# Kernel optimization log

Hardware: AMD Instinct MI355X
Metric: run time of the kernel (lower is better)

## Reference

```python
import jax, jax.numpy as jnp
import numpy as np

T = 4096       # sentence length
E = 256        # embedding_dim
H = 512        # hidden_dim (bidirectional total)
HD = H // 2    # per-direction hidden
V = 100000     # vocab_size
NT = 16        # tagset_size
START, STOP = 14, 15
NEG = -10000.0


def setup_inputs() -> dict:
    key = jax.random.key(0)
    ks = jax.random.split(key, 20)
    sentence = jax.random.randint(ks[0], (T,), 0, V)
    emb = jax.random.normal(ks[1], (V, E), dtype=jnp.float32)
    # PyTorch LSTM params: gate order [i, f, g, o], weight_ih [4*HD, E], weight_hh [4*HD, HD]
    s = 1.0 / np.sqrt(HD)
    def U(k, shape):
        return jax.random.uniform(k, shape, dtype=jnp.float32, minval=-s, maxval=s)
    Wih_f, Whh_f = U(ks[2], (4 * HD, E)), U(ks[3], (4 * HD, HD))
    bih_f, bhh_f = U(ks[4], (4 * HD,)), U(ks[5], (4 * HD,))
    Wih_b, Whh_b = U(ks[6], (4 * HD, E)), U(ks[7], (4 * HD, HD))
    bih_b, bhh_b = U(ks[8], (4 * HD,)), U(ks[9], (4 * HD,))
    h0 = jax.random.normal(ks[10], (2, 1, HD), dtype=jnp.float32)  # init_hidden()
    c0 = jax.random.normal(ks[11], (2, 1, HD), dtype=jnp.float32)
    # attention params (zeros in the original; small randn for a non-degenerate baseline)
    w_omega = jax.random.normal(ks[12], (H, H), dtype=jnp.float32) * 0.01
    u_omega = jax.random.normal(ks[13], (H,), dtype=jnp.float32) * 0.01
    sl = 1.0 / np.sqrt(H)
    W_tag = jax.random.uniform(ks[14], (NT, H), dtype=jnp.float32, minval=-sl, maxval=sl)
    b_tag = jax.random.uniform(ks[15], (NT,), dtype=jnp.float32, minval=-sl, maxval=sl)
    transitions = jax.random.normal(ks[16], (NT, NT), dtype=jnp.float32)
    transitions = transitions.at[START, :].set(NEG).at[:, STOP].set(NEG)
    return dict(sentence=sentence, emb=emb,
                Wih_f=Wih_f, Whh_f=Whh_f, bih_f=bih_f, bhh_f=bhh_f,
                Wih_b=Wih_b, Whh_b=Whh_b, bih_b=bih_b, bhh_b=bhh_b,
                h0=h0, c0=c0, w_omega=w_omega, u_omega=u_omega,
                W_tag=W_tag, b_tag=b_tag, transitions=transitions)


def _lstm_dir(x, h0, c0, Wih, Whh, bih, bhh, reverse):
    # x: [T, E]; returns hidden states [T, HD]
    def step(carry, xt):
        h, c = carry
        g = xt @ Wih.T + h @ Whh.T + bih + bhh  # [4*HD]
        i, f, gg, o = jnp.split(g, 4)
        i, f, o = jax.nn.sigmoid(i), jax.nn.sigmoid(f), jax.nn.sigmoid(o)
        c = f * c + i * jnp.tanh(gg)
        h = o * jnp.tanh(c)
        return (h, c), h
    _, hs = jax.lax.scan(step, (h0, c0), x, reverse=reverse)
    return hs


def _lstm_feats(sentence, emb, Wih_f, Whh_f, bih_f, bhh_f,
                Wih_b, Whh_b, bih_b, bhh_b, h0, c0,
                w_omega, u_omega, W_tag, b_tag):
    x = emb[sentence]  # [T, E]
    hf = _lstm_dir(x, h0[0, 0], c0[0, 0], Wih_f, Whh_f, bih_f, bhh_f, False)
    hb = _lstm_dir(x, h0[1, 0], c0[1, 0], Wih_b, Whh_b, bih_b, bhh_b, True)
    out = jnp.concatenate([hf, hb], axis=-1)  # [T, H] (lstm_out with batch=1 squeezed)
    # attention_net: softmax over time of a scalar score per position
    logits = jnp.tanh(out @ w_omega) @ u_omega  # [T]
    alphas = jax.nn.softmax(logits)
    attn_out = out * alphas[:, None]  # [T, H]
    return attn_out @ W_tag.T + b_tag  # [T, NT]


def _viterbi(feats, transitions):
    init = jnp.full((NT,), NEG, dtype=feats.dtype).at[START].set(0.0)
    def step(fv, feat):
        scores = fv[None, :] + transitions  # [next_tag, prev_tag]
        bp = jnp.argmax(scores, axis=1)
        return jnp.max(scores, axis=1) + feat, bp
    fv, bps = jax.lax.scan(step, init, feats)
    terminal = fv + transitions[STOP]
    best = jnp.argmax(terminal)
    score = terminal[best]
    def back(tag, bp):
        return bp[tag], tag
    _, path = jax.lax.scan(back, best, bps, reverse=True)  # path[t] = best tag at t
    return score, path


def reference(sentence, emb, Wih_f, Whh_f, bih_f, bhh_f,
              Wih_b, Whh_b, bih_b, bhh_b, h0, c0,
              w_omega, u_omega, W_tag, b_tag, transitions):
    feats = _lstm_feats(sentence, emb, Wih_f, Whh_f, bih_f, bhh_f,
                        Wih_b, Whh_b, bih_b, bhh_b, h0, c0,
                        w_omega, u_omega, W_tag, b_tag)
    score, path = _viterbi(feats, transitions)
    return score, path
```

## Files before the change

kernel.cpp:

```cpp
#include <hip/hip_runtime.h>
#include <hip/hip_fp16.h>

#define T_LEN 4096
#define START_TAG 14
#define STOP_TAG 15
#define NEG_VAL -10000.0f

typedef unsigned int u32;
typedef unsigned short u16;
typedef unsigned long long u64;
typedef int v4i __attribute__((ext_vector_type(4)));

#define GX_OFF      0u
#define OUT_OFF     16777216u
#define LOGITS_OFF  25165824u
#define ALPHAS_OFF  25182208u
#define FEATS_OFF   25198592u
#define CMAT_OFF    25460736u
#define VIN_OFF     25591808u
#define BP_OFF      25600000u
#define BMAP_OFF    25632768u
#define STAIL_OFF   25640960u
#define BEST_OFF    25649152u

__device__ __forceinline__ u32 packq(int q0, int q1, int q2, int q3) {
  return (u32)(q0 & 255) | ((u32)(q1 & 255) << 8) |
         ((u32)(q2 & 255) << 16) | ((u32)(q3 & 255) << 24);
}

__device__ __forceinline__ float sigm(float x) {
  return __builtin_amdgcn_rcpf(1.f + __expf(-x));
}
__device__ __forceinline__ float tanh_fast(float x) {
  float e = __expf(-2.f * fabsf(x));
  float r = (1.f - e) * __builtin_amdgcn_rcpf(1.f + e);
  return copysignf(r, x);
}

__global__ void prep_kernel(float* logits) {
  const int i = threadIdx.x + blockIdx.x * 1024;
  if (i < 4096) logits[i] = 0.f;
}

__global__ __launch_bounds__(256) void gx_kernel(
    const int* __restrict__ sentence, const float* __restrict__ emb,
    const float* __restrict__ Wih_f, const float* __restrict__ Wih_b,
    const float* __restrict__ bih_f, const float* __restrict__ bhh_f,
    const float* __restrict__ bih_b, const float* __restrict__ bhh_b,
    __half* __restrict__ Gx)
{
  __shared__ float ws[32][260];
  const int r0 = blockIdx.x * 32;
  const int t0 = blockIdx.y * 32;
  const int tid = threadIdx.x;
  {
    const int c4 = (tid & 63) * 4;
    const int rA = tid >> 6;
    #pragma unroll
    for (int p = 0; p < 8; ++p) {
      const int rr = rA + p * 4;
      const int R = r0 + rr;
      const float* src = (R < 1024) ? (Wih_f + (size_t)R * 256 + c4)
                                    : (Wih_b + (size_t)(R - 1024) * 256 + c4);
      *(float4*)&ws[rr][c4] = *(const float4*)src;
    }
  }
  __syncthreads();
  const int ttb = tid >> 4, rgb = tid & 15;
  const int s0r = sentence[t0 + ttb];
  const int s1r = sentence[t0 + ttb + 16];
  const float* x0p = emb + (size_t)s0r * 256;
  const float* x1p = emb + (size_t)s1r * 256;
  float acc00 = 0, acc01 = 0, acc10 = 0, acc11 = 0;
  #pragma unroll 4
  for (int c4 = 0; c4 < 256; c4 += 4) {
    float4 x0 = *(const float4*)(x0p + c4);
    float4 x1 = *(const float4*)(x1p + c4);
    float4 w0 = *(const float4*)&ws[rgb][c4];
    float4 w1 = *(const float4*)&ws[rgb + 16][c4];
    acc00 += x0.x*w0.x + x0.y*w0.y + x0.z*w0.z + x0.w*w0.w;
    acc01 += x0.x*w1.x + x0.y*w1.y + x0.z*w1.z + x0.w*w1.w;
    acc10 += x1.x*w0.x + x1.y*w0.y + x1.z*w0.z + x1.w*w0.w;
    acc11 += x1.x*w1.x + x1.y*w1.y + x1.z*w1.z + x1.w*w1.w;
  }
  #pragma unroll
  for (int ri = 0; ri < 2; ++ri) {
    const int R = r0 + rgb + ri * 16;
    const int dir = R >> 10, grow = R & 1023;
    const int gate = grow >> 8, dd = grow & 255;
    const float bias = dir ? (bih_b[grow] + bhh_b[grow])
                           : (bih_f[grow] + bhh_f[grow]);
    const float a0 = ri ? acc01 : acc00;
    const float a1 = ri ? acc11 : acc10;
    const size_t off = (size_t)dir * 1024 + dd * 4 + gate;
    Gx[(size_t)(t0 + ttb) * 2048 + off]      = __float2half(a0 + bias);
    Gx[(size_t)(t0 + ttb + 16) * 2048 + off] = __float2half(a1 + bias);
  }
}

__global__ __launch_bounds__(512, 2) void lstm_kernel(
    const float* __restrict__ Whh_f, const float* __restrict__ Whh_b,
    const float* __restrict__ h0, const float* __restrict__ c0,
    const __half* __restrict__ Gx, float* __restrict__ out_lstm)
{
  const int dir = blockIdx.x;
  const int tid = threadIdx.x;
  const int w = tid >> 6, l = tid & 63;
  const int mr = l & 15, q = l >> 4;
  const float* Whh = dir ? Whh_b : Whh_f;

  __shared__ __align__(16) char hq8[2][256];
  __shared__ __align__(16) int graw[1024];
  __shared__ float fsh[1024];
  __shared__ __align__(16) u16 hist[128 * 256];

  v4i wfrag[8][4];
  #pragma unroll
  for (int m = 0; m < 8; ++m) {
    const int row = 128 * w + 16 * m + mr;
    const float* wr = Whh + (size_t)row * 256 + 16 * q;
    float mx = 1e-10f;
    #pragma unroll
    for (int t = 0; t < 4; ++t) {
      #pragma unroll
      for (int c4 = 0; c4 < 4; ++c4) {
        float4 f = *(const float4*)(wr + 64 * t + 4 * c4);
        mx = fmaxf(mx, fmaxf(fmaxf(fabsf(f.x), fabsf(f.y)),
                             fmaxf(fabsf(f.z), fabsf(f.w))));
      }
    }
    mx = fmaxf(mx, __shfl_xor(mx, 16));
    mx = fmaxf(mx, __shfl_xor(mx, 32));
    const float qs = 127.f / mx;
    if (q == 0) fsh[row] = mx * (1.f / (127.f * 32.f));
    #pragma unroll
    for (int t = 0; t < 4; ++t) {
      u32 pk[4];
      #pragma unroll
      for (int c4 = 0; c4 < 4; ++c4) {
        float4 f = *(const float4*)(wr + 64 * t + 4 * c4);
        pk[c4] = packq((int)rintf(f.x * qs), (int)rintf(f.y * qs),
                       (int)rintf(f.z * qs), (int)rintf(f.w * qs));
      }
      v4i v; v[0] = (int)pk[0]; v[1] = (int)pk[1]; v[2] = (int)pk[2]; v[3] = (int)pk[3];
      wfrag[m][t] = v;
    }
  }

  float creg = 0.f;
  if (tid < 256) {
    creg = c0[dir * 256 + tid];
    float hv = h0[dir * 256 + tid];
    int qq = max(-127, min(127, (int)rintf(hv * 32.f)));
    hq8[0][tid] = (char)qq;
  }
  __syncthreads();

  float fsi = 0.f, fsf = 0.f, fsg = 0.f, fso = 0.f;
  if (tid < 256) {
    fsi = fsh[tid]; fsf = fsh[256 + tid];
    fsg = fsh[512 + tid]; fso = fsh[768 + tid];
  }
  const uint2* Gx2 = (const uint2*)Gx;

  for (int sb = 0; sb < T_LEN; sb += 16) {
    uint2 gb[16];
    if (tid < 256) {
      #pragma unroll
      for (int k = 0; k < 16; ++k) {
        const int t = dir ? (T_LEN - 1 - (sb + k)) : (sb + k);
        gb[k] = Gx2[(size_t)t * 512 + dir * 256 + tid];
      }
    }
    #pragma unroll
    for (int k = 0; k < 16; ++k) {
      const int s = sb + k;
      const char* hc = hq8[k & 1];
      v4i bfr[4];
      #pragma unroll
      for (int t = 0; t < 4; ++t)
        bfr[t] = *(const v4i*)(hc + 64 * t + 16 * q);
      #pragma unroll
      for (int m = 0; m < 8; ++m) {
        v4i acc; acc[0] = 0; acc[1] = 0; acc[2] = 0; acc[3] = 0;
        acc = __builtin_amdgcn_mfma_i32_16x16x64_i8(wfrag[m][0], bfr[0], acc, 0, 0, 0);
        acc = __builtin_amdgcn_mfma_i32_16x16x64_i8(wfrag[m][1], bfr[1], acc, 0, 0, 0);
        acc = __builtin_amdgcn_mfma_i32_16x16x64_i8(wfrag[m][2], bfr[2], acc, 0, 0, 0);
        acc = __builtin_amdgcn_mfma_i32_16x16x64_i8(wfrag[m][3], bfr[3], acc, 0, 0, 0);
        if (mr == 0)
          *(v4i*)&graw[128 * w + 16 * m + 4 * q] = acc;
      }
      __syncthreads();
      if (tid < 256) {
        const int d = tid;
        const int ri = graw[d],        rf = graw[256 + d];
        const int rg = graw[512 + d],  ro = graw[768 + d];
        const float xi = (float)ri * fsi + __half2float(__ushort_as_half((u16)(gb[k].x & 0xffff)));
        const float xf = (float)rf * fsf + __half2float(__ushort_as_half((u16)(gb[k].x >> 16)));
        const float xg = (float)rg * fsg + __half2float(__ushort_as_half((u16)(gb[k].y & 0xffff)));
        const float xo = (float)ro * fso + __half2float(__ushort_as_half((u16)(gb[k].y >> 16)));
        const float iv = sigm(xi);
        const float fv = sigm(xf);
        const float gv = tanh_fast(xg);
        const float ov = sigm(xo);
        creg = __builtin_fmaf(fv, creg, iv * gv);
        const float h = ov * tanh_fast(creg);
        hist[(s & 127) * 256 + d] = __half_as_ushort(__float2half(h));
        int qq = max(-127, min(127, (int)rintf(h * 32.f)));
        hq8[(k + 1) & 1][d] = (char)qq;
      }
      __syncthreads();
      if ((s & 127) == 127) {
        const int sbase = s - 127;
        #pragma unroll 4
        for (int i = 0; i < 16; ++i) {
          const int idx = tid + i * 512;
          const int step = idx >> 6, d0 = (idx & 63) * 4;
          const int tt = sbase + step;
          const int tg = dir ? (T_LEN - 1 - tt) : tt;
          uint2 hv = ((const uint2*)hist)[idx];
          float4 ov4;
          ov4.x = __half2float(__ushort_as_half((u16)(hv.x & 0xffff)));
          ov4.y = __half2float(__ushort_as_half((u16)(hv.x >> 16)));
          ov4.z = __half2float(__ushort_as_half((u16)(hv.y & 0xffff)));
          ov4.w = __half2float(__ushort_as_half((u16)(hv.y >> 16)));
          *(float4*)&out_lstm[(size_t)tg * 512 + dir * 256 + d0] = ov4;
        }
        __syncthreads();
      }
    }
  }
}

__global__ __launch_bounds__(256) void attn_kernel(
    const float* __restrict__ out_lstm, const float* __restrict__ w_omega,
    const float* __restrict__ u_omega, float* __restrict__ logits)
{
  __shared__ float bst[32][132];
  const int c0 = blockIdx.x * 32;
  const int t0 = blockIdx.y * 32;
  const int tid = threadIdx.x;
  const int ttb = tid >> 4, cgb = tid & 15;
  const float* a0p = out_lstm + (size_t)(t0 + ttb) * 512;
  const float* a1p = out_lstm + (size_t)(t0 + ttb + 16) * 512;
  float acc00 = 0, acc01 = 0, acc10 = 0, acc11 = 0;
  for (int kh = 0; kh < 4; ++kh) {
    __syncthreads();
    {
      const int cc = tid & 31;
      const int kA = tid >> 5;
      #pragma unroll
      for (int p = 0; p < 16; ++p) {
        const int kkx = kA + p * 8;
        bst[cc][kkx] = w_omega[(size_t)(kh * 128 + kkx) * 512 + c0 + cc];
      }
    }
    __syncthreads();
    #pragma unroll 4
    for (int k4 = 0; k4 < 128; k4 += 4) {
      float4 a0 = *(const float4*)(a0p + kh * 128 + k4);
      float4 a1 = *(const float4*)(a1p + kh * 128 + k4);
      float4 b0 = *(const float4*)&bst[cgb][k4];
      float4 b1 = *(const float4*)&bst[cgb + 16][k4];
      acc00 += a0.x*b0.x + a0.y*b0.y + a0.z*b0.z + a0.w*b0.w;
      acc01 += a0.x*b1.x + a0.y*b1.y + a0.z*b1.z + a0.w*b1.w;
      acc10 += a1.x*b0.x + a1.y*b0.y + a1.z*b0.z + a1.w*b0.w;
      acc11 += a1.x*b1.x + a1.y*b1.y + a1.z*b1.z + a1.w*b1.w;
    }
  }
  const float u0 = u_omega[c0 + cgb], u1 = u_omega[c0 + 16 + cgb];
  float s0 = tanh_fast(acc00) * u0 + tanh_fast(acc01) * u1;
  float s1 = tanh_fast(acc10) * u0 + tanh_fast(acc11) * u1;
  #pragma unroll
  for (int msk = 1; msk < 16; msk <<= 1) {
    s0 += __shfl_xor(s0, msk);
    s1 += __shfl_xor(s1, msk);
  }
  if (cgb == 0) {
    atomicAdd(&logits[t0 + ttb], s0);
    atomicAdd(&logits[t0 + ttb + 16], s1);
  }
}

__global__ __launch_bounds__(1024) void softmax_kernel(
    const float* __restrict__ logits, float* __restrict__ alphas)
{
  __shared__ float red[1024];
  const int tid = threadIdx.x;
  float l0 = logits[tid], l1 = logits[1024 + tid];
  float l2 = logits[2048 + tid], l3 = logits[3072 + tid];
  red[tid] = fmaxf(fmaxf(l0, l1), fmaxf(l2, l3));
  __syncthreads();
  for (int s = 512; s > 0; s >>= 1) {
    if (tid < s) red[tid] = fmaxf(red[tid], red[tid + s]);
    __syncthreads();
  }
  const float gm = red[0];
  __syncthreads();
  float e0 = __expf(l0 - gm), e1 = __expf(l1 - gm);
  float e2 = __expf(l2 - gm), e3 = __expf(l3 - gm);
  red[tid] = e0 + e1 + e2 + e3;
  __syncthreads();
  for (int s = 512; s > 0; s >>= 1) {
    if (tid < s) red[tid] += red[tid + s];
    __syncthreads();
  }
  const float inv = 1.0f / red[0];
  alphas[tid] = e0 * inv; alphas[1024 + tid] = e1 * inv;
  alphas[2048 + tid] = e2 * inv; alphas[3072 + tid] = e3 * inv;
}

__global__ __launch_bounds__(256) void feats_kernel(
    const float* __restrict__ out_lstm, const float* __restrict__ W_tag,
    const float* __restrict__ b_tag, const float* __restrict__ alphas,
    float* __restrict__ feats)
{
  __shared__ float wt[16][516];
  const int t0 = blockIdx.x * 16;
  const int tid = threadIdx.x;
  {
    const int k4 = (tid & 127) * 4;
    const int gA = tid >> 7;
    #pragma unroll
    for (int p = 0; p < 8; ++p) {
      const int tg = gA + p * 2;
      *(float4*)&wt[tg][k4] = *(const float4*)(W_tag + (size_t)tg * 512 + k4);
    }
  }
  __syncthreads();
  const int tt = tid >> 4, tg = tid & 15;
  const float* ap = out_lstm + (size_t)(t0 + tt) * 512;
  float acc = 0.f;
  #pragma unroll 4
  for (int k4 = 0; k4 < 512; k4 += 4) {
    float4 a = *(const float4*)(ap + k4);
    float4 b = *(const float4*)&wt[tg][k4];
    acc += a.x*b.x + a.y*b.y + a.z*b.z + a.w*b.w;
  }
  feats[(size_t)(t0 + tt) * 16 + tg] = acc * alphas[t0 + tt] + b_tag[tg];
}

__global__ __launch_bounds__(256) void vit_block_mats(
    const float* __restrict__ feats, const float* __restrict__ trans,
    float* __restrict__ Cmat)
{
  __shared__ float C[2][16][17];
  const int b = blockIdx.x;
  const int tid = threadIdx.x;
  const int n = tid >> 4, p = tid & 15;
  float tr[16];
  #pragma unroll
  for (int k = 0; k < 16; ++k) tr[k] = trans[n * 16 + k];
  const int t0 = b * 32;
  C[0][n][p] = tr[p] + feats[t0 * 16 + n];
  float fnext = feats[(t0 + 1) * 16 + n];
  __syncthreads();
  for (int s = 1; s < 32; ++s) {
    const float ft = fnext;
    if (s + 1 < 32) fnext = feats[(t0 + s + 1) * 16 + n];
    const int pr = (s - 1) & 1, cu = s & 1;
    float m = tr[0] + C[pr][0][p];
    #pragma unroll
    for (int k = 1; k < 16; ++k) m = fmaxf(m, tr[k] + C[pr][k][p]);
    C[cu][n][p] = m + ft;
    __syncthreads();
  }
  Cmat[b * 256 + n * 16 + p] = C[1][n][p];
}

__global__ __launch_bounds__(64) void vit_scan(
    const float* __restrict__ Cmat, const float* __restrict__ trans,
    float* __restrict__ v_in, float* __restrict__ d_out, u32* __restrict__ best_ws)
{
  const int l = threadIdx.x;
  const int n = l & 15, pg = l >> 4;
  float v = (n == START_TAG) ? 0.f : NEG_VAL;
  for (int b = 0; b < 128; ++b) {
    if (pg == 0) v_in[b * 16 + n] = v;
    float4 c4 = *(const float4*)&Cmat[b * 256 + n * 16 + pg * 4];
    float cand = c4.x + __shfl(v, pg * 4 + 0);
    cand = fmaxf(cand, c4.y + __shfl(v, pg * 4 + 1));
    cand = fmaxf(cand, c4.z + __shfl(v, pg * 4 + 2));
    cand = fmaxf(cand, c4.w + __shfl(v, pg * 4 + 3));
    cand = fmaxf(cand, __shfl_xor(cand, 16));
    cand = fmaxf(cand, __shfl_xor(cand, 32));
    v = cand;
  }
  float term = v + trans[STOP_TAG * 16 + n];
  int mi = n;
  #pragma unroll
  for (int msk = 1; msk < 16; msk <<= 1) {
    float om = __shfl_xor(term, msk); int omi = __shfl_xor(mi, msk);
    if (om > term || (om == term && omi < mi)) { term = om; mi = omi; }
  }
  if (l == 0) { d_out[0] = term; *best_ws = (u32)mi; }
}

__global__ __launch_bounds__(64) void vit_bp(
    const float* __restrict__ feats, const float* __restrict__ trans,
    const float* __restrict__ v_in, u32* __restrict__ bp)
{
  const int b = blockIdx.x;
  const int l = threadIdx.x;
  const int n = l & 15, pg = l >> 4;
  const float4 tr4 = *(const float4*)&trans[n * 16 + pg * 4];
  float v = v_in[b * 16 + n];
  const int t0 = b * 32;
  float fcur = feats[t0 * 16 + n];
  for (int s = 0; s < 32; ++s) {
    const int t = t0 + s;
    float fnext = (s + 1 < 32) ? feats[(t + 1) * 16 + n] : 0.f;
    float f0 = __shfl(v, pg * 4 + 0), f1 = __shfl(v, pg * 4 + 1);
    float f2 = __shfl(v, pg * 4 + 2), f3 = __shfl(v, pg * 4 + 3);
    float m = f0 + tr4.x; int mi = pg * 4;
    float c;
    c = f1 + tr4.y; if (c > m) { m = c; mi = pg * 4 + 1; }
    c = f2 + tr4.z; if (c > m) { m = c; mi = pg * 4 + 2; }
    c = f3 + tr4.w; if (c > m) { m = c; mi = pg * 4 + 3; }
    float om; int omi;
    om = __shfl_xor(m, 16); omi = __shfl_xor(mi, 16);
    if (om > m || (om == m && omi < mi)) { m = om; mi = omi; }
    om = __shfl_xor(m, 32); omi = __shfl_xor(mi, 32);
    if (om > m || (om == m && omi < mi)) { m = om; mi = omi; }
    u32 w = (l < 16) ? ((u32)mi << ((n & 7) * 4)) : 0u;
    w |= __shfl_xor(w, 1); w |= __shfl_xor(w, 2); w |= __shfl_xor(w, 4);
    if (l == 0) bp[t * 2] = w;
    if (l == 8) bp[t * 2 + 1] = w;
    v = m + fcur;
    fcur = fnext;
  }
}

__global__ __launch_bounds__(64) void vit_bmap(
    const u32* __restrict__ bp, u32* __restrict__ Bmap)
{
  const int b = blockIdx.x;
  const int l = threadIdx.x;
  if (l >= 16) return;
  int t = b * 32 + 31;
  u32 lo = bp[t * 2], hi = bp[t * 2 + 1];
  int A = (int)(((l < 8 ? lo : hi) >> ((l & 7) * 4)) & 15u);
  for (t = b * 32 + 30; t >= b * 32; --t) {
    lo = bp[t * 2]; hi = bp[t * 2 + 1];
    A = (int)(((A < 8 ? lo : hi) >> ((A & 7) * 4)) & 15u);
  }
  Bmap[b * 16 + l] = (u32)A;
}

__global__ __launch_bounds__(64) void vit_suffix(
    const u32* __restrict__ Bmap, u32* __restrict__ Stail)
{
  __shared__ u32 bm[2048];
  const int l = threadIdx.x;
  for (int i = l; i < 2048; i += 64) bm[i] = Bmap[i];
  __syncthreads();
  if (l < 16) {
    int S = l;
    for (int b = 127; b >= 0; --b) {
      Stail[b * 16 + l] = (u32)S;
      S = (int)bm[b * 16 + S];
    }
  }
}

__global__ __launch_bounds__(64) void vit_emit(
    const u32* __restrict__ bp, const u32* __restrict__ Stail,
    const u32* __restrict__ best_ws, float* __restrict__ d_out)
{
  const int b = blockIdx.x;
  const int l = threadIdx.x;
  const int best = (int)*best_ws;
  int A = (l < 16) ? (int)Stail[b * 16 + l] : 0;
  for (int s = 31; s >= 0; --s) {
    const int t = b * 32 + s;
    const int pv = __shfl(A, best);
    if (l == 0) d_out[1 + t] = (float)pv;
    if (s > 0) {
      const u32 lo = bp[t * 2], hi = bp[t * 2 + 1];
      A = (int)(((A < 8 ? lo : hi) >> ((A & 7) * 4)) & 15u);
    }
  }
}

extern "C" void kernel_launch(void* const* d_in, const int* in_sizes, int n_in,
                              void* d_out, int out_size, void* d_ws, size_t ws_size,
                              hipStream_t stream)
{
  const int*   sentence = (const int*)  d_in[0];
  const float* emb      = (const float*)d_in[1];
  const float* Wih_f    = (const float*)d_in[2];
  const float* Whh_f    = (const float*)d_in[3];
  const float* bih_f    = (const float*)d_in[4];
  const float* bhh_f    = (const float*)d_in[5];
  const float* Wih_b    = (const float*)d_in[6];
  const float* Whh_b    = (const float*)d_in[7];
  const float* bih_b    = (const float*)d_in[8];
  const float* bhh_b    = (const float*)d_in[9];
  const float* h0       = (const float*)d_in[10];
  const float* c0       = (const float*)d_in[11];
  const float* w_omega  = (const float*)d_in[12];
  const float* u_omega  = (const float*)d_in[13];
  const float* W_tag    = (const float*)d_in[14];
  const float* b_tag    = (const float*)d_in[15];
  const float* trans    = (const float*)d_in[16];

  char* ws = (char*)d_ws;
  __half* Gx      = (__half*)(ws + GX_OFF);
  float* out_lstm = (float*)(ws + OUT_OFF);
  float* logits   = (float*)(ws + LOGITS_OFF);
  float* alphas   = (float*)(ws + ALPHAS_OFF);
  float* feats    = (float*)(ws + FEATS_OFF);
  float* Cmat     = (float*)(ws + CMAT_OFF);
  float* v_in     = (float*)(ws + VIN_OFF);
  u32*   bp       = (u32*)  (ws + BP_OFF);
  u32*   Bmap     = (u32*)  (ws + BMAP_OFF);
  u32*   Stail    = (u32*)  (ws + STAIL_OFF);
  u32*   best_ws  = (u32*)  (ws + BEST_OFF);
  float* out      = (float*)d_out;

  hipLaunchKernelGGL(prep_kernel, dim3(4), dim3(1024), 0, stream, logits);
  hipLaunchKernelGGL(gx_kernel, dim3(64, 128), dim3(256), 0, stream,
                     sentence, emb, Wih_f, Wih_b, bih_f, bhh_f, bih_b, bhh_b, Gx);
  hipLaunchKernelGGL(lstm_kernel, dim3(2), dim3(512), 0, stream,
                     Whh_f, Whh_b, h0, c0, Gx, out_lstm);
  hipLaunchKernelGGL(attn_kernel, dim3(16, 128), dim3(256), 0, stream,
                     out_lstm, w_omega, u_omega, logits);
  hipLaunchKernelGGL(softmax_kernel, dim3(1), dim3(1024), 0, stream, logits, alphas);
  hipLaunchKernelGGL(feats_kernel, dim3(256), dim3(256), 0, stream,
                     out_lstm, W_tag, b_tag, alphas, feats);
  hipLaunchKernelGGL(vit_block_mats, dim3(128), dim3(256), 0, stream,
                     feats, trans, Cmat);
  hipLaunchKernelGGL(vit_scan, dim3(1), dim3(64), 0, stream,
                     Cmat, trans, v_in, out, best_ws);
  hipLaunchKernelGGL(vit_bp, dim3(128), dim3(64), 0, stream,
                     feats, trans, v_in, bp);
  hipLaunchKernelGGL(vit_bmap, dim3(128), dim3(64), 0, stream, bp, Bmap);
  hipLaunchKernelGGL(vit_suffix, dim3(1), dim3(64), 0, stream, Bmap, Stail);
  hipLaunchKernelGGL(vit_emit, dim3(128), dim3(64), 0, stream,
                     bp, Stail, best_ws, out);
}
```

Measured before the change: 4.076 ms.

## Split LSTM gates: MFMA for i/f, per-thread sdot4 for g/o with 256 threads

The recurrent LSTM kernel drops from 512 to 256 threads per direction. The i and f gate matvecs still run on int8 MFMA. The g and o gate rows are quantized into per-thread registers (128 ints) and computed with sdot4 dot products over the broadcast h vector. Gx prefetch is double-buffered in chunks of 8 steps, and the barriers use a custom s_barrier with an explicit lgkmcnt wait. The aim is to cut barrier cost with fewer waves and overlap the MFMA work with scalar dot work, but the large per-thread register arrays risk spills and longer serial dot chains.

```diff
diff --git a/kernel.cpp b/kernel.cpp
--- a/kernel.cpp
+++ b/kernel.cpp
@@ -35,6 +35,27 @@
   float e = __expf(-2.f * fabsf(x));
   float r = (1.f - e) * __builtin_amdgcn_rcpf(1.f + e);
   return copysignf(r, x);
+}
+
+#if defined(__has_builtin)
+#  if __has_builtin(__builtin_amdgcn_sdot4)
+#    define DOT4(a, b, c) __builtin_amdgcn_sdot4((a), (b), (c), false)
+#  endif
+#endif
+#ifndef DOT4
+__device__ __forceinline__ int dot4_emu(int a, int b, int c) {
+  #pragma unroll
+  for (int j = 0; j < 4; ++j)
+    c += (int)((signed char)(a >> (8 * j))) * (int)((signed char)(b >> (8 * j)));
+  return c;
+}
+#  define DOT4(a, b, c) dot4_emu((a), (b), (c))
+#endif
+
+__device__ __forceinline__ void wg_barrier() {
+  asm volatile("s_waitcnt lgkmcnt(0)" ::: "memory");
+  __builtin_amdgcn_s_barrier();
+  __builtin_amdgcn_sched_barrier(0);
 }
 
 __global__ void prep_kernel(float* logits) {
@@ -98,20 +119,21 @@
   }
 }
 
-__global__ __launch_bounds__(512, 2) void lstm_kernel(
+__global__ __launch_bounds__(256, 1) void lstm_kernel(
     const float* __restrict__ Whh_f, const float* __restrict__ Whh_b,
     const float* __restrict__ h0, const float* __restrict__ c0,
     const __half* __restrict__ Gx, float* __restrict__ out_lstm)
 {
   const int dir = blockIdx.x;
   const int tid = threadIdx.x;
+  const int d = tid;
   const int w = tid >> 6, l = tid & 63;
   const int mr = l & 15, q = l >> 4;
   const float* Whh = dir ? Whh_b : Whh_f;
 
   __shared__ __align__(16) char hq8[2][256];
-  __shared__ __align__(16) int graw[1024];
-  __shared__ float fsh[1024];
+  __shared__ __align__(16) int graw[512];
+  __shared__ float fsh[512];
   __shared__ __align__(16) u16 hist[128 * 256];
 
   v4i wfrag[8][4];
@@ -147,39 +169,68 @@
     }
   }
 
-  float creg = 0.f;
-  if (tid < 256) {
-    creg = c0[dir * 256 + tid];
-    float hv = h0[dir * 256 + tid];
+  int wq2[2][64];
+  float fsg = 0.f, fso = 0.f;
+  #pragma unroll
+  for (int g = 0; g < 2; ++g) {
+    const float* wr = Whh + (size_t)((2 + g) * 256 + d) * 256;
+    float mx = 1e-10f;
+    #pragma unroll
+    for (int c4 = 0; c4 < 64; ++c4) {
+      float4 f = *(const float4*)(wr + c4 * 4);
+      mx = fmaxf(mx, fmaxf(fmaxf(fabsf(f.x), fabsf(f.y)),
+                           fmaxf(fabsf(f.z), fabsf(f.w))));
+    }
+    const float qs = 127.f / mx;
+    const float sc = mx * (1.f / (127.f * 32.f));
+    if (g == 0) fsg = sc; else fso = sc;
+    #pragma unroll
+    for (int c4 = 0; c4 < 64; ++c4) {
+      float4 f = *(const float4*)(wr + c4 * 4);
+      wq2[g][c4] = (int)packq((int)rintf(f.x * qs), (int)rintf(f.y * qs),
+                              (int)rintf(f.z * qs), (int)rintf(f.w * qs));
+    }
+  }
+
+  float creg = c0[dir * 256 + d];
+  {
+    float hv = h0[dir * 256 + d];
     int qq = max(-127, min(127, (int)rintf(hv * 32.f)));
-    hq8[0][tid] = (char)qq;
-  }
-  __syncthreads();
-
-  float fsi = 0.f, fsf = 0.f, fsg = 0.f, fso = 0.f;
-  if (tid < 256) {
-    fsi = fsh[tid]; fsf = fsh[256 + tid];
-    fsg = fsh[512 + tid]; fso = fsh[768 + tid];
-  }
+    hq8[0][d] = (char)qq;
+  }
+  __syncthreads();
+
+  const float fsi = fsh[d], fsf = fsh[256 + d];
   const uint2* Gx2 = (const uint2*)Gx;
-
-  for (int sb = 0; sb < T_LEN; sb += 16) {
-    uint2 gb[16];
-    if (tid < 256) {
-      #pragma unroll
-      for (int k = 0; k < 16; ++k) {
-        const int t = dir ? (T_LEN - 1 - (sb + k)) : (sb + k);
-        gb[k] = Gx2[(size_t)t * 512 + dir * 256 + tid];
-      }
-    }
-    #pragma unroll
-    for (int k = 0; k < 16; ++k) {
+  uint2 ga[8];
+  #pragma unroll
+  for (int k = 0; k < 8; ++k) {
+    const int t = dir ? (T_LEN - 1 - k) : k;
+    ga[k] = Gx2[(size_t)t * 512 + dir * 256 + d];
+  }
+
+  for (int sb = 0; sb < T_LEN; sb += 8) {
+    uint2 gn[8];
+    const bool more = (sb + 8) < T_LEN;
+    if (more) {
+      #pragma unroll
+      for (int k = 0; k < 8; ++k) {
+        const int t2 = sb + 8 + k;
+        const int t = dir ? (T_LEN - 1 - t2) : t2;
+        gn[k] = Gx2[(size_t)t * 512 + dir * 256 + d];
+      }
+    }
+    #pragma unroll
+    for (int k = 0; k < 8; ++k) {
       const int s = sb + k;
-      const char* hc = hq8[k & 1];
+      const char* hc = hq8[s & 1];
       v4i bfr[4];
       #pragma unroll
       for (int t = 0; t < 4; ++t)
         bfr[t] = *(const v4i*)(hc + 64 * t + 16 * q);
+      int4 hv[16];
+      #pragma unroll
+      for (int c = 0; c < 16; ++c) hv[c] = ((const int4*)hc)[c];
       #pragma unroll
       for (int m = 0; m < 8; ++m) {
         v4i acc; acc[0] = 0; acc[1] = 0; acc[2] = 0; acc[3] = 0;
@@ -190,44 +241,60 @@
         if (mr == 0)
           *(v4i*)&graw[128 * w + 16 * m + 4 * q] = acc;
       }
-      __syncthreads();
-      if (tid < 256) {
-        const int d = tid;
-        const int ri = graw[d],        rf = graw[256 + d];
-        const int rg = graw[512 + d],  ro = graw[768 + d];
-        const float xi = (float)ri * fsi + __half2float(__ushort_as_half((u16)(gb[k].x & 0xffff)));
-        const float xf = (float)rf * fsf + __half2float(__ushort_as_half((u16)(gb[k].x >> 16)));
-        const float xg = (float)rg * fsg + __half2float(__ushort_as_half((u16)(gb[k].y & 0xffff)));
-        const float xo = (float)ro * fso + __half2float(__ushort_as_half((u16)(gb[k].y >> 16)));
-        const float iv = sigm(xi);
-        const float fv = sigm(xf);
-        const float gv = tanh_fast(xg);
-        const float ov = sigm(xo);
-        creg = __builtin_fmaf(fv, creg, iv * gv);
-        const float h = ov * tanh_fast(creg);
-        hist[(s & 127) * 256 + d] = __half_as_ushort(__float2half(h));
+      int ag0 = 0, ag1 = 0, ao0 = 0, ao1 = 0;
+      #pragma unroll
+      for (int c = 0; c < 16; ++c) {
+        const int4 h4 = hv[c];
+        ag0 = DOT4(wq2[0][4*c+0], h4.x, ag0);
+        ao0 = DOT4(wq2[1][4*c+0], h4.x, ao0);
+        ag1 = DOT4(wq2[0][4*c+1], h4.y, ag1);
+        ao1 = DOT4(wq2[1][4*c+1], h4.y, ao1);
+        ag0 = DOT4(wq2[0][4*c+2], h4.z, ag0);
+        ao0 = DOT4(wq2[1][4*c+2], h4.z, ao0);
+        ag1 = DOT4(wq2[0][4*c+3], h4.w, ag1);
+        ao1 = DOT4(wq2[1][4*c+3], h4.w, ao1);
+      }
+      const int ag = ag0 + ag1, ao = ao0 + ao1;
+      wg_barrier();
+      const int ri = graw[d], rf = graw[256 + d];
+      const float xi = (float)ri * fsi + __half2float(__ushort_as_half((u16)(ga[k].x & 0xffff)));
+      const float xf = (float)rf * fsf + __half2float(__ushort_as_half((u16)(ga[k].x >> 16)));
+      const float xg = (float)ag * fsg + __half2float(__ushort_as_half((u16)(ga[k].y & 0xffff)));
+      const float xo = (float)ao * fso + __half2float(__ushort_as_half((u16)(ga[k].y >> 16)));
+      const float iv = sigm(xi);
+      const float fv = sigm(xf);
+      const float gv = tanh_fast(xg);
+      const float ov = sigm(xo);
+      creg = __builtin_fmaf(fv, creg, iv * gv);
+      const float h = ov * tanh_fast(creg);
+      {
         int qq = max(-127, min(127, (int)rintf(h * 32.f)));
-        hq8[(k + 1) & 1][d] = (char)qq;
-      }
-      __syncthreads();
-      if ((s & 127) == 127) {
-        const int sbase = s - 127;
-        #pragma unroll 4
-        for (int i = 0; i < 16; ++i) {
-          const int idx = tid + i * 512;
-          const int step = idx >> 6, d0 = (idx & 63) * 4;
-          const int tt = sbase + step;
-          const int tg = dir ? (T_LEN - 1 - tt) : tt;
-          uint2 hv = ((const uint2*)hist)[idx];
-          float4 ov4;
-          ov4.x = __half2float(__ushort_as_half((u16)(hv.x & 0xffff)));
-          ov4.y = __half2float(__ushort_as_half((u16)(hv.x >> 16)));
-          ov4.z = __half2float(__ushort_as_half((u16)(hv.y & 0xffff)));
-          ov4.w = __half2float(__ushort_as_half((u16)(hv.y >> 16)));
-          *(float4*)&out_lstm[(size_t)tg * 512 + dir * 256 + d0] = ov4;
-        }
-        __syncthreads();
-      }
+        hq8[(s + 1) & 1][d] = (char)qq;
+      }
+      hist[(s & 127) * 256 + d] = __half_as_ushort(__float2half(h));
+      wg_barrier();
+    }
+    if ((sb & 127) == 120) {
+      const int sbase = sb - 120;
+      #pragma unroll 4
+      for (int i = 0; i < 32; ++i) {
+        const int idx = tid + i * 256;
+        const int step = idx >> 6, d0 = (idx & 63) * 4;
+        const int tt = sbase + step;
+        const int tg = dir ? (T_LEN - 1 - tt) : tt;
+        uint2 hv = ((const uint2*)hist)[idx];
+        float4 ov4;
+        ov4.x = __half2float(__ushort_as_half((u16)(hv.x & 0xffff)));
+        ov4.y = __half2float(__ushort_as_half((u16)(hv.x >> 16)));
+        ov4.z = __half2float(__ushort_as_half((u16)(hv.y & 0xffff)));
+        ov4.w = __half2float(__ushort_as_half((u16)(hv.y >> 16)));
+        *(float4*)&out_lstm[(size_t)tg * 512 + dir * 256 + d0] = ov4;
+      }
+      wg_barrier();
+    }
+    if (more) {
+      #pragma unroll
+      for (int k = 0; k < 8; ++k) ga[k] = gn[k];
     }
   }
 }
@@ -521,7 +588,7 @@
   hipLaunchKernelGGL(prep_kernel, dim3(4), dim3(1024), 0, stream, logits);
   hipLaunchKernelGGL(gx_kernel, dim3(64, 128), dim3(256), 0, stream,
                      sentence, emb, Wih_f, Wih_b, bih_f, bhh_f, bih_b, bhh_b, Gx);
-  hipLaunchKernelGGL(lstm_kernel, dim3(2), dim3(512), 0, stream,
+  hipLaunchKernelGGL(lstm_kernel, dim3(2), dim3(256), 0, stream,
                      Whh_f, Whh_b, h0, c0, Gx, out_lstm);
   hipLaunchKernelGGL(attn_kernel, dim3(16, 128), dim3(256), 0, stream,
                      out_lstm, w_omega, u_omega, logits);
```

Result: slower. 5.650 ms (+38.6%).

## Remap LSTM gate rows per wave to drop a barrier per timestep

Applied to the files above, without the earlier changes.

Reorders the recurrent weight rows so each wave computes all four gates for its own 32 hidden units. The cell update can then read gate results after a wave-local LDS fence instead of a workgroup barrier, which removes one of the two block-wide syncs per step. It also double-buffers the Gx prefetch in 8-step chunks so the global loads overlap compute, and uses custom barrier intrinsics. The cost is a more intricate index mapping and only 32 active lanes per wave in the elementwise phase.

```diff
diff --git a/kernel.cpp b/kernel.cpp
--- a/kernel.cpp
+++ b/kernel.cpp
@@ -35,6 +35,16 @@
   float e = __expf(-2.f * fabsf(x));
   float r = (1.f - e) * __builtin_amdgcn_rcpf(1.f + e);
   return copysignf(r, x);
+}
+
+__device__ __forceinline__ void wg_barrier() {
+  asm volatile("s_waitcnt lgkmcnt(0)" ::: "memory");
+  __builtin_amdgcn_s_barrier();
+  __builtin_amdgcn_sched_barrier(0);
+}
+__device__ __forceinline__ void wave_lds_fence() {
+  asm volatile("s_waitcnt lgkmcnt(0)" ::: "memory");
+  __builtin_amdgcn_sched_barrier(0);
 }
 
 __global__ void prep_kernel(float* logits) {
@@ -110,14 +120,14 @@
   const float* Whh = dir ? Whh_b : Whh_f;
 
   __shared__ __align__(16) char hq8[2][256];
-  __shared__ __align__(16) int graw[1024];
+  __shared__ __align__(16) int graw[8][128];
   __shared__ float fsh[1024];
   __shared__ __align__(16) u16 hist[128 * 256];
 
   v4i wfrag[8][4];
   #pragma unroll
   for (int m = 0; m < 8; ++m) {
-    const int row = 128 * w + 16 * m + mr;
+    const int row = (m & 3) * 256 + 32 * w + 16 * (m >> 2) + mr;
     const float* wr = Whh + (size_t)row * 256 + 16 * q;
     float mx = 1e-10f;
     #pragma unroll
@@ -147,35 +157,47 @@
     }
   }
 
+  const int d = 32 * w + (l & 31);
   float creg = 0.f;
-  if (tid < 256) {
-    creg = c0[dir * 256 + tid];
-    float hv = h0[dir * 256 + tid];
+  if (l < 32) {
+    creg = c0[dir * 256 + d];
+    float hv = h0[dir * 256 + d];
     int qq = max(-127, min(127, (int)rintf(hv * 32.f)));
-    hq8[0][tid] = (char)qq;
-  }
-  __syncthreads();
-
-  float fsi = 0.f, fsf = 0.f, fsg = 0.f, fso = 0.f;
-  if (tid < 256) {
-    fsi = fsh[tid]; fsf = fsh[256 + tid];
-    fsg = fsh[512 + tid]; fso = fsh[768 + tid];
+    hq8[0][d] = (char)qq;
+  }
+  __syncthreads();
+
+  float fs0 = 0.f, fs1 = 0.f, fs2 = 0.f, fs3 = 0.f;
+  if (l < 32) {
+    fs0 = fsh[d]; fs1 = fsh[256 + d]; fs2 = fsh[512 + d]; fs3 = fsh[768 + d];
   }
   const uint2* Gx2 = (const uint2*)Gx;
-
-  for (int sb = 0; sb < T_LEN; sb += 16) {
-    uint2 gb[16];
-    if (tid < 256) {
-      #pragma unroll
-      for (int k = 0; k < 16; ++k) {
-        const int t = dir ? (T_LEN - 1 - (sb + k)) : (sb + k);
-        gb[k] = Gx2[(size_t)t * 512 + dir * 256 + tid];
-      }
-    }
-    #pragma unroll
-    for (int k = 0; k < 16; ++k) {
+  uint2 ga[8];
+  if (l < 32) {
+    #pragma unroll
+    for (int k = 0; k < 8; ++k) {
+      const int t = dir ? (T_LEN - 1 - k) : k;
+      ga[k] = Gx2[(size_t)t * 512 + dir * 256 + d];
+    }
+  }
+
+  const int hb = (l & 31) >> 4, li = l & 15;
+
+  for (int sb = 0; sb < T_LEN; sb += 8) {
+    uint2 gn[8];
+    const bool more = (sb + 8) < T_LEN;
+    if (more && l < 32) {
+      #pragma unroll
+      for (int k = 0; k < 8; ++k) {
+        const int t2 = sb + 8 + k;
+        const int t = dir ? (T_LEN - 1 - t2) : t2;
+        gn[k] = Gx2[(size_t)t * 512 + dir * 256 + d];
+      }
+    }
+    #pragma unroll
+    for (int k = 0; k < 8; ++k) {
       const int s = sb + k;
-      const char* hc = hq8[k & 1];
+      const char* hc = hq8[s & 1];
       v4i bfr[4];
       #pragma unroll
       for (int t = 0; t < 4; ++t)
@@ -188,46 +210,51 @@
         acc = __builtin_amdgcn_mfma_i32_16x16x64_i8(wfrag[m][2], bfr[2], acc, 0, 0, 0);
         acc = __builtin_amdgcn_mfma_i32_16x16x64_i8(wfrag[m][3], bfr[3], acc, 0, 0, 0);
         if (mr == 0)
-          *(v4i*)&graw[128 * w + 16 * m + 4 * q] = acc;
-      }
-      __syncthreads();
-      if (tid < 256) {
-        const int d = tid;
-        const int ri = graw[d],        rf = graw[256 + d];
-        const int rg = graw[512 + d],  ro = graw[768 + d];
-        const float xi = (float)ri * fsi + __half2float(__ushort_as_half((u16)(gb[k].x & 0xffff)));
-        const float xf = (float)rf * fsf + __half2float(__ushort_as_half((u16)(gb[k].x >> 16)));
-        const float xg = (float)rg * fsg + __half2float(__ushort_as_half((u16)(gb[k].y & 0xffff)));
-        const float xo = (float)ro * fso + __half2float(__ushort_as_half((u16)(gb[k].y >> 16)));
+          *(v4i*)&graw[w][(m & 3) * 32 + (m >> 2) * 16 + 4 * q] = acc;
+      }
+      wave_lds_fence();
+      if (l < 32) {
+        const int ri = graw[w][       hb * 16 + li];
+        const int rf = graw[w][ 32 +  hb * 16 + li];
+        const int rg = graw[w][ 64 +  hb * 16 + li];
+        const int ro = graw[w][ 96 +  hb * 16 + li];
+        const float xi = (float)ri * fs0 + __half2float(__ushort_as_half((u16)(ga[k].x & 0xffff)));
+        const float xf = (float)rf * fs1 + __half2float(__ushort_as_half((u16)(ga[k].x >> 16)));
+        const float xg = (float)rg * fs2 + __half2float(__ushort_as_half((u16)(ga[k].y & 0xffff)));
+        const float xo = (float)ro * fs3 + __half2float(__ushort_as_half((u16)(ga[k].y >> 16)));
         const float iv = sigm(xi);
         const float fv = sigm(xf);
         const float gv = tanh_fast(xg);
         const float ov = sigm(xo);
         creg = __builtin_fmaf(fv, creg, iv * gv);
         const float h = ov * tanh_fast(creg);
+        int qq = max(-127, min(127, (int)rintf(h * 32.f)));
+        hq8[(s + 1) & 1][d] = (char)qq;
         hist[(s & 127) * 256 + d] = __half_as_ushort(__float2half(h));
-        int qq = max(-127, min(127, (int)rintf(h * 32.f)));
-        hq8[(k + 1) & 1][d] = (char)qq;
-      }
-      __syncthreads();
-      if ((s & 127) == 127) {
-        const int sbase = s - 127;
-        #pragma unroll 4
-        for (int i = 0; i < 16; ++i) {
-          const int idx = tid + i * 512;
-          const int step = idx >> 6, d0 = (idx & 63) * 4;
-          const int tt = sbase + step;
-          const int tg = dir ? (T_LEN - 1 - tt) : tt;
-          uint2 hv = ((const uint2*)hist)[idx];
-          float4 ov4;
-          ov4.x = __half2float(__ushort_as_half((u16)(hv.x & 0xffff)));
-          ov4.y = __half2float(__ushort_as_half((u16)(hv.x >> 16)));
-          ov4.z = __half2float(__ushort_as_half((u16)(hv.y & 0xffff)));
-          ov4.w = __half2float(__ushort_as_half((u16)(hv.y >> 16)));
-          *(float4*)&out_lstm[(size_t)tg * 512 + dir * 256 + d0] = ov4;
-        }
-        __syncthreads();
-      }
+      }
+      wg_barrier();
+    }
+    if ((sb & 127) == 120) {
+      const int sbase = sb - 120;
+      #pragma unroll 4
+      for (int i = 0; i < 16; ++i) {
+        const int idx = tid + i * 512;
+        const int step = idx >> 6, d0 = (idx & 63) * 4;
+        const int tt = sbase + step;
+        const int tg = dir ? (T_LEN - 1 - tt) : tt;
+        uint2 hv = ((const uint2*)hist)[idx];
+        float4 ov4;
+        ov4.x = __half2float(__ushort_as_half((u16)(hv.x & 0xffff)));
+        ov4.y = __half2float(__ushort_as_half((u16)(hv.x >> 16)));
+        ov4.z = __half2float(__ushort_as_half((u16)(hv.y & 0xffff)));
+        ov4.w = __half2float(__ushort_as_half((u16)(hv.y >> 16)));
+        *(float4*)&out_lstm[(size_t)tg * 512 + dir * 256 + d0] = ov4;
+      }
+      wg_barrier();
+    }
+    if (more && l < 32) {
+      #pragma unroll
+      for (int k = 0; k < 8; ++k) ga[k] = gn[k];
     }
   }
 }
```

Result: slower. 4.453 ms (+9.3%).
